# Kernel tuning notes

Hardware: AMD Instinct MI355X
Metric: run time of the kernel (lower is better)

## Reference

```python
import jax, jax.numpy as jnp
import numpy as np

B, NC, H, W, NT = 8, 2048, 128, 128, 4096
EPS = 1e-6


def _off_grid_interp(pts, vals, q):
    """Piecewise-linear scattered interpolation (Delaunay surrogate).
    pts: (Nc,2), vals: (Nc,1), q: (Nt,2) -> (Nt,1).
    For each query, take the 3 nearest context points, compute barycentric
    weights in that triangle; outside/degenerate falls back to mean fill,
    mirroring LinearNDInterpolator(fill_value=vals.mean()).
    """
    d2 = jnp.sum((q[:, None, :] - pts[None, :, :]) ** 2, axis=-1)  # (Nt, Nc)
    _, idx = jax.lax.top_k(-d2, 3)                                  # (Nt, 3)
    tri = pts[idx]                                                  # (Nt, 3, 2)
    tv = vals[idx]                                                  # (Nt, 3, 1)
    p0 = tri[:, 0]
    e1 = tri[:, 1] - p0
    e2 = tri[:, 2] - p0
    r = q - p0
    det = e1[:, 0] * e2[:, 1] - e1[:, 1] * e2[:, 0]
    det_safe = jnp.where(jnp.abs(det) < EPS, 1.0, det)
    w1 = (r[:, 0] * e2[:, 1] - r[:, 1] * e2[:, 0]) / det_safe
    w2 = (e1[:, 0] * r[:, 1] - e1[:, 1] * r[:, 0]) / det_safe
    w0 = 1.0 - w1 - w2
    inside = (w0 >= -EPS) & (w1 >= -EPS) & (w2 >= -EPS) & (jnp.abs(det) >= EPS)
    interp = (w0[:, None] * tv[:, 0] + w1[:, None] * tv[:, 1]
              + w2[:, None] * tv[:, 2])                             # (Nt, 1)
    fill = jnp.mean(vals)
    return jnp.where(inside[:, None], interp, fill)


def _on_grid_interp(grid_x, grid_y, vals, q):
    """Bilinear interpolation on a rectilinear grid (scipy.interpolate.interpn,
    method='linear', bounds_error=False, fill_value=vals.mean()).
    grid_x: (H,), grid_y: (W,), vals: (H,W,1), q: (Nt,2) -> (Nt,1).
    """
    qx, qy = q[:, 0], q[:, 1]
    ix = jnp.clip(jnp.searchsorted(grid_x, qx) - 1, 0, grid_x.shape[0] - 2)
    iy = jnp.clip(jnp.searchsorted(grid_y, qy) - 1, 0, grid_y.shape[0] - 2)
    tx = ((qx - grid_x[ix]) / (grid_x[ix + 1] - grid_x[ix]))[:, None]
    ty = ((qy - grid_y[iy]) / (grid_y[iy + 1] - grid_y[iy]))[:, None]
    v00 = vals[ix, iy]
    v01 = vals[ix, iy + 1]
    v10 = vals[ix + 1, iy]
    v11 = vals[ix + 1, iy + 1]
    interp = (v00 * (1 - tx) * (1 - ty) + v10 * tx * (1 - ty)
              + v01 * (1 - tx) * ty + v11 * tx * ty)
    inside = ((qx >= grid_x[0]) & (qx <= grid_x[-1])
              & (qy >= grid_y[0]) & (qy <= grid_y[-1]))
    fill = jnp.mean(vals)
    return jnp.where(inside[:, None], interp, fill)


def setup_inputs() -> dict:
    key = jax.random.key(0)
    ks = jax.random.split(key, 6)
    xc_off_grid = jax.random.uniform(ks[0], (B, NC, 2), minval=-1.0, maxval=1.0)
    yc_off_grid = jax.random.normal(ks[1], (B, NC, 1))
    gx = jnp.linspace(-1.0, 1.0, H)
    gy = jnp.linspace(-1.0, 1.0, W)
    grid = jnp.stack(jnp.meshgrid(gx, gy, indexing='ij'), axis=-1)  # (H,W,2)
    xc_on_grid = jnp.broadcast_to(grid, (B, H, W, 2))
    yc_on_grid = jax.random.normal(ks[2], (B, H, W, 1))
    xt = jax.random.uniform(ks[3], (B, NT, 2), minval=-1.0, maxval=1.0)
    mix_w = jax.random.normal(ks[4], (2, 1)) * 0.5
    mix_b = jax.random.normal(ks[5], (1,)) * 0.1
    return dict(xc_off_grid=xc_off_grid, yc_off_grid=yc_off_grid,
                xc_on_grid=xc_on_grid, yc_on_grid=yc_on_grid, xt=xt,
                mix_w=mix_w, mix_b=mix_b)


def reference(xc_off_grid, yc_off_grid, xc_on_grid, yc_on_grid, xt, mix_w, mix_b):
    # off-grid scattered interpolation, vmapped over batch
    yt_off = jax.vmap(_off_grid_interp)(xc_off_grid, yc_off_grid, xt)  # (B,Nt,1)
    # on-grid: axis coordinates exactly as the original (bxc_on[:,0,0], bxc_on[0,:,1])
    gx = xc_on_grid[:, :, 0, 0]  # (B, H)
    gy = xc_on_grid[:, 0, :, 1]  # (B, W)
    yt_on = jax.vmap(_on_grid_interp)(gx, gy, yc_on_grid, xt)          # (B,Nt,1)
    yt = jnp.concatenate([yt_off, yt_on], axis=-1)                     # (B,Nt,2)
    return yt @ mix_w + mix_b                                          # (B,Nt,1)
```

## Files before the change

### kernel.cpp

```cpp
#include <hip/hip_runtime.h>
#include <math.h>

#define NB   8
#define NC   2048
#define HH   128
#define WW   128
#define NTQ  4096
#define EPSF 1e-6f
#define CELLW 0.125f
#define BLK  512
#define QPB  64
#define LPQ  8
#define UMAX 0xFFFFFFFFFFFFFFFFULL

typedef unsigned long long u64;

__device__ __forceinline__ void ins3u(u64 u, u64& U0, u64& U1, u64& U2) {
    bool lt2 = u < U2, lt1 = u < U1, lt0 = u < U0;
    U2 = lt1 ? U1 : (lt2 ? u : U2);
    U1 = lt0 ? U0 : (lt1 ? u : U1);
    U0 = lt0 ? u  : U0;
}

__global__ __launch_bounds__(BLK) void fused_interp_kernel(
    const float* __restrict__ xc_off,
    const float* __restrict__ yc_off,
    const float* __restrict__ xc_on,
    const float* __restrict__ yc_on,
    const float* __restrict__ xt,
    const float* __restrict__ mw,
    const float* __restrict__ mb,
    float* __restrict__ out)
{
#pragma clang fp contract(off)
    __shared__ float4 spts[NC];
    __shared__ int    shist[256];
    __shared__ int    soffs[257];
    __shared__ int    scur[256];
    __shared__ float  sgx[HH];
    __shared__ float  sgy[WW];
    __shared__ float  sred[8];
    __shared__ int4   sres[QPB];

    const int tid   = threadIdx.x;
    const int b     = blockIdx.x >> 6;
    const int qbase = (blockIdx.x & 63) * QPB;

    if (tid < 256) shist[tid] = 0;
    const float* xob = xc_on + (size_t)b * HH * WW * 2;
    if (tid >= 256 && tid < 256 + HH) sgx[tid - 256] = xob[(size_t)(tid - 256) * (WW * 2)];
    if (tid >= 384 && tid < 384 + WW) sgy[tid - 384] = xob[2 * (tid - 384) + 1];
    __syncthreads();

    const float2* xcb = (const float2*)(xc_off + (size_t)b * NC * 2);
    const float*  ycb = yc_off + (size_t)b * NC;
    float2 pp_[4]; float vv_[4]; int cc_[4];
    float vsum = 0.f;
#pragma unroll
    for (int t = 0; t < 4; ++t) {
        int k = tid + t * BLK;
        float2 P = xcb[k];
        float  V = ycb[k];
        pp_[t] = P; vv_[t] = V;
        int cx = (int)floorf((P.x + 1.0f) * 8.0f); cx = min(max(cx, 0), 15);
        int cy = (int)floorf((P.y + 1.0f) * 8.0f); cy = min(max(cy, 0), 15);
        cc_[t] = cy * 16 + cx;
        atomicAdd(&shist[cc_[t]], 1);
        vsum += V;
    }
    for (int o = 32; o > 0; o >>= 1) vsum += __shfl_down(vsum, o);
    if ((tid & 63) == 0) sred[tid >> 6] = vsum;
    __syncthreads();

    if (tid < 64) {
        int h0 = shist[4*tid], h1 = shist[4*tid+1], h2 = shist[4*tid+2], h3 = shist[4*tid+3];
        int s = h0 + h1 + h2 + h3; int tot = s;
        for (int off = 1; off < 64; off <<= 1) {
            int u = __shfl_up(s, off);
            if (tid >= off) s += u;
        }
        int excl = s - tot;
        soffs[4*tid]   = excl;
        soffs[4*tid+1] = excl + h0;
        soffs[4*tid+2] = excl + h0 + h1;
        soffs[4*tid+3] = excl + h0 + h1 + h2;
        if (tid == 63) soffs[256] = excl + tot;
    }
    __syncthreads();
    if (tid < 256) scur[tid] = soffs[tid];
    __syncthreads();

#pragma unroll
    for (int t = 0; t < 4; ++t) {
        int k = tid + t * BLK;
        int pos = atomicAdd(&scur[cc_[t]], 1);
        float4 o4; o4.x = pp_[t].x; o4.y = pp_[t].y; o4.z = vv_[t]; o4.w = __int_as_float(k);
        spts[pos] = o4;
    }
    __syncthreads();

    const float fillv = (sred[0] + sred[1] + sred[2] + sred[3] +
                         sred[4] + sred[5] + sred[6] + sred[7]) / (float)NC;

    const int g   = tid & (LPQ - 1);
    const int grp = tid >> 3;
    const int q   = qbase + grp;
    const float2 Q = ((const float2*)xt)[(size_t)b * NTQ + q];
    const float qx = Q.x, qy = Q.y;
    int qcx = (int)floorf((qx + 1.0f) * 8.0f); qcx = min(max(qcx, 0), 15);
    int qcy = (int)floorf((qy + 1.0f) * 8.0f); qcy = min(max(qcy, 0), 15);

    u64 P0 = UMAX, P1 = UMAX, P2 = UMAX;
    u64 F0 = UMAX, F1 = UMAX, F2 = UMAX;

    for (int row = 0; row < 3; ++row) {
        int cy = qcy + row - 1;
        if (cy < 0 || cy > 15) continue;
        int c0 = cy * 16 + max(qcx - 1, 0);
        int c1 = cy * 16 + min(qcx + 1, 15);
        int s = soffs[c0], e = soffs[c1 + 1];
        for (int k = s + g; k < e; k += LPQ) {
            float4 P = spts[k];
            float dx = qx - P.x, dy = qy - P.y;
            float dd = dx * dx + dy * dy;
            u64 u = ((u64)__float_as_uint(dd) << 32) | (unsigned int)__float_as_int(P.w);
            ins3u(u, F0, F1, F2);
        }
    }
    for (int m = 1; m <= 4; m <<= 1) {
        u64 e0 = __shfl_xor(F0, m), e1 = __shfl_xor(F1, m), e2 = __shfl_xor(F2, m);
        ins3u(e0, F0, F1, F2);
        ins3u(e1, F0, F1, F2);
        ins3u(e2, F0, F1, F2);
    }
    P0 = F0; P1 = F1; P2 = F2;

    float bnd = 1.0f * CELLW - 1e-6f;
    u64 thr = ((u64)__float_as_uint(bnd * bnd)) << 32;
    bool done = P2 < thr;

    for (int r = 2; r <= 15; ++r) {
        if (__all(done)) break;
        if (!done) {
            F0 = F1 = F2 = UMAX;
            for (int t = g; t < 8 * r; t += LPQ) {
                int side = t / (2 * r), u = t % (2 * r);
                int dx, dy;
                if (side == 0)      { dx = -r + u; dy = -r; }
                else if (side == 1) { dx = r;      dy = -r + u; }
                else if (side == 2) { dx = r - u;  dy = r; }
                else                { dx = -r;     dy = r - u; }
                int cx = qcx + dx, cy = qcy + dy;
                if (cx < 0 || cx > 15 || cy < 0 || cy > 15) continue;
                int c = cy * 16 + cx;
                int s = soffs[c], e = soffs[c + 1];
                for (int k = s; k < e; ++k) {
                    float4 P = spts[k];
                    float ddx = qx - P.x, ddy = qy - P.y;
                    float dd = ddx * ddx + ddy * ddy;
                    u64 uu = ((u64)__float_as_uint(dd) << 32) | (unsigned int)__float_as_int(P.w);
                    ins3u(uu, F0, F1, F2);
                }
            }
            for (int m = 1; m <= 4; m <<= 1) {
                u64 e0 = __shfl_xor(F0, m), e1 = __shfl_xor(F1, m), e2 = __shfl_xor(F2, m);
                ins3u(e0, F0, F1, F2);
                ins3u(e1, F0, F1, F2);
                ins3u(e2, F0, F1, F2);
            }
            ins3u(F0, P0, P1, P2);
            ins3u(F1, P0, P1, P2);
            ins3u(F2, P0, P1, P2);
            float bb = (float)r * CELLW - 1e-6f;
            u64 tt = ((u64)__float_as_uint(bb * bb)) << 32;
            done = P2 < tt;
        }
    }

    if (g == 0) {
        int4 r4;
        r4.x = (int)(P0 & 0xFFFFFFFFULL);
        r4.y = (int)(P1 & 0xFFFFFFFFULL);
        r4.z = (int)(P2 & 0xFFFFFFFFULL);
        r4.w = 0;
        sres[grp] = r4;
    }
    __syncthreads();

    if (tid < QPB) {
        const int4 r4 = sres[tid];
        const int J0 = r4.x, J1 = r4.y, J2 = r4.z;
        const float2 Qe = ((const float2*)xt)[(size_t)b * NTQ + qbase + tid];
        const float ex = Qe.x, ey = Qe.y;

        float2 A  = xcb[J0];
        float2 Bp = xcb[J1];
        float2 C  = xcb[J2];
        float e1x = Bp.x - A.x, e1y = Bp.y - A.y;
        float e2x = C.x  - A.x, e2y = C.y  - A.y;
        float rx  = ex - A.x,   ry  = ey - A.y;
        float det = e1x * e2y - e1y * e2x;
        float adet = fabsf(det);
        float dets = (adet < EPSF) ? 1.0f : det;
        float w1 = (rx * e2y - ry * e2x) / dets;
        float w2 = (e1x * ry - e1y * rx) / dets;
        float w0 = 1.0f - w1 - w2;
        bool inside = (w0 >= -EPSF) && (w1 >= -EPSF) && (w2 >= -EPSF) && (adet >= EPSF);
        float interp = w0 * ycb[J0] + w1 * ycb[J1] + w2 * ycb[J2];
        float yoff = inside ? interp : fillv;

        int ix = (int)((ex + 1.0f) * 63.5f);
        ix = min(max(ix, 0), HH - 2);
        while (ix > 0 && !(sgx[ix] < ex)) --ix;
        while (ix < HH - 2 && sgx[ix + 1] < ex) ++ix;
        int iy = (int)((ey + 1.0f) * 63.5f);
        iy = min(max(iy, 0), WW - 2);
        while (iy > 0 && !(sgy[iy] < ey)) --iy;
        while (iy < WW - 2 && sgy[iy + 1] < ey) ++iy;

        float x0 = sgx[ix], x1 = sgx[ix + 1];
        float y0 = sgy[iy], y1 = sgy[iy + 1];
        float tx = (ex - x0) / (x1 - x0);
        float ty = (ey - y0) / (y1 - y0);
        const float* yob = yc_on + (size_t)b * HH * WW;
        float v00 = yob[ix * WW + iy];
        float v01 = yob[ix * WW + iy + 1];
        float v10 = yob[(ix + 1) * WW + iy];
        float v11 = yob[(ix + 1) * WW + iy + 1];
        float yon = v00 * (1.f - tx) * (1.f - ty)
                  + v10 * tx * (1.f - ty)
                  + v01 * (1.f - tx) * ty
                  + v11 * tx * ty;

        out[(size_t)b * NTQ + qbase + tid] = yoff * mw[0] + yon * mw[1] + mb[0];
    }
}

extern "C" void kernel_launch(void* const* d_in, const int* in_sizes, int n_in,
                              void* d_out, int out_size, void* d_ws, size_t ws_size,
                              hipStream_t stream) {
    const float* xc_off = (const float*)d_in[0];
    const float* yc_off = (const float*)d_in[1];
    const float* xc_on  = (const float*)d_in[2];
    const float* yc_on  = (const float*)d_in[3];
    const float* xt     = (const float*)d_in[4];
    const float* mix_w  = (const float*)d_in[5];
    const float* mix_b  = (const float*)d_in[6];
    float* out = (float*)d_out;

    fused_interp_kernel<<<NB * (NTQ / QPB), BLK, 0, stream>>>(
        xc_off, yc_off, xc_on, yc_on, xt, mix_w, mix_b, out);
}
```

Baseline: 13.73 us.

## Split grid-binning build into separate kernel, share sorted points via workspace

```diff
diff --git a/kernel.cpp b/kernel.cpp
--- a/kernel.cpp
+++ b/kernel.cpp
@@ -15,6 +15,11 @@
 
 typedef unsigned long long u64;
 
+#define WS_PTS  0
+#define WS_OFF  (NB * NC * 16)
+#define WS_MEAN (WS_OFF + NB * 257 * 4)
+#define WS_NEED (WS_MEAN + NB * 4)
+
 __device__ __forceinline__ void ins3u(u64 u, u64& U0, u64& U1, u64& U2) {
     bool lt2 = u < U2, lt1 = u < U1, lt0 = u < U0;
     U2 = lt1 ? U1 : (lt2 ? u : U2);
@@ -22,43 +27,28 @@
     U0 = lt0 ? u  : U0;
 }
 
-__global__ __launch_bounds__(BLK) void fused_interp_kernel(
-    const float* __restrict__ xc_off,
-    const float* __restrict__ yc_off,
-    const float* __restrict__ xc_on,
-    const float* __restrict__ yc_on,
-    const float* __restrict__ xt,
-    const float* __restrict__ mw,
-    const float* __restrict__ mb,
-    float* __restrict__ out)
+__global__ __launch_bounds__(1024) void build_kernel(
+    const float* __restrict__ xc_off, const float* __restrict__ yc_off,
+    float4* __restrict__ wpts, int* __restrict__ woffs, float* __restrict__ wmean)
 {
-#pragma clang fp contract(off)
     __shared__ float4 spts[NC];
     __shared__ int    shist[256];
     __shared__ int    soffs[257];
     __shared__ int    scur[256];
-    __shared__ float  sgx[HH];
-    __shared__ float  sgy[WW];
-    __shared__ float  sred[8];
-    __shared__ int4   sres[QPB];
-
-    const int tid   = threadIdx.x;
-    const int b     = blockIdx.x >> 6;
-    const int qbase = (blockIdx.x & 63) * QPB;
-
+    __shared__ float  sred[16];
+
+    const int tid = threadIdx.x;
+    const int b   = blockIdx.x;
     if (tid < 256) shist[tid] = 0;
-    const float* xob = xc_on + (size_t)b * HH * WW * 2;
-    if (tid >= 256 && tid < 256 + HH) sgx[tid - 256] = xob[(size_t)(tid - 256) * (WW * 2)];
-    if (tid >= 384 && tid < 384 + WW) sgy[tid - 384] = xob[2 * (tid - 384) + 1];
     __syncthreads();
 
     const float2* xcb = (const float2*)(xc_off + (size_t)b * NC * 2);
     const float*  ycb = yc_off + (size_t)b * NC;
-    float2 pp_[4]; float vv_[4]; int cc_[4];
+    float2 pp_[2]; float vv_[2]; int cc_[2];
     float vsum = 0.f;
 #pragma unroll
-    for (int t = 0; t < 4; ++t) {
-        int k = tid + t * BLK;
+    for (int t = 0; t < 2; ++t) {
+        int k = tid + t * 1024;
         float2 P = xcb[k];
         float  V = ycb[k];
         pp_[t] = P; vv_[t] = V;
@@ -91,16 +81,54 @@
     __syncthreads();
 
 #pragma unroll
-    for (int t = 0; t < 4; ++t) {
-        int k = tid + t * BLK;
+    for (int t = 0; t < 2; ++t) {
+        int k = tid + t * 1024;
         int pos = atomicAdd(&scur[cc_[t]], 1);
         float4 o4; o4.x = pp_[t].x; o4.y = pp_[t].y; o4.z = vv_[t]; o4.w = __int_as_float(k);
         spts[pos] = o4;
     }
     __syncthreads();
 
-    const float fillv = (sred[0] + sred[1] + sred[2] + sred[3] +
-                         sred[4] + sred[5] + sred[6] + sred[7]) / (float)NC;
+#pragma unroll
+    for (int t = 0; t < 2; ++t) {
+        int i = tid + t * 1024;
+        wpts[(size_t)b * NC + i] = spts[i];
+    }
+    if (tid < 257) woffs[b * 257 + tid] = soffs[tid];
+    if (tid == 0) {
+        float s = 0.f;
+        for (int i = 0; i < 16; ++i) s += sred[i];
+        wmean[b] = s / (float)NC;
+    }
+}
+
+__global__ __launch_bounds__(BLK) void search_kernel(
+    const float4* __restrict__ wpts, const int* __restrict__ woffs,
+    const float* __restrict__ wmean,
+    const float* __restrict__ xc_off, const float* __restrict__ yc_off,
+    const float* __restrict__ xc_on,  const float* __restrict__ yc_on,
+    const float* __restrict__ xt, const float* __restrict__ mw,
+    const float* __restrict__ mb, float* __restrict__ out)
+{
+#pragma clang fp contract(off)
+    __shared__ float4 spts[NC];
+    __shared__ int    soffs[257];
+    __shared__ float  sgx[HH];
+    __shared__ float  sgy[WW];
+    __shared__ int4   sres[QPB];
+
+    const int tid   = threadIdx.x;
+    const int b     = blockIdx.x >> 6;
+    const int qbase = (blockIdx.x & 63) * QPB;
+
+    const float4* wp = wpts + (size_t)b * NC;
+#pragma unroll
+    for (int i = tid; i < NC; i += BLK) spts[i] = wp[i];
+    if (tid < 257) soffs[tid] = woffs[b * 257 + tid];
+    const float* xob = xc_on + (size_t)b * HH * WW * 2;
+    if (tid >= 288 && tid < 288 + HH) sgx[tid - 288] = xob[(size_t)(tid - 288) * (WW * 2)];
+    if (tid >= 384 && tid < 384 + WW) sgy[tid - 384] = xob[2 * (tid - 384) + 1];
+    __syncthreads();
 
     const int g   = tid & (LPQ - 1);
     const int grp = tid >> 3;
@@ -188,6 +216,9 @@
     __syncthreads();
 
     if (tid < QPB) {
+        const float fillv = wmean[b];
+        const float2* xcb = (const float2*)(xc_off + (size_t)b * NC * 2);
+        const float*  ycb = yc_off + (size_t)b * NC;
         const int4 r4 = sres[tid];
         const int J0 = r4.x, J1 = r4.y, J2 = r4.z;
         const float2 Qe = ((const float2*)xt)[(size_t)b * NTQ + qbase + tid];
@@ -236,6 +267,188 @@
     }
 }
 
+__global__ __launch_bounds__(BLK) void fused_interp_kernel(
+    const float* __restrict__ xc_off, const float* __restrict__ yc_off,
+    const float* __restrict__ xc_on,  const float* __restrict__ yc_on,
+    const float* __restrict__ xt, const float* __restrict__ mw,
+    const float* __restrict__ mb, float* __restrict__ out)
+{
+#pragma clang fp contract(off)
+    __shared__ float4 spts[NC];
+    __shared__ int    shist[256];
+    __shared__ int    soffs[257];
+    __shared__ int    scur[256];
+    __shared__ float  sgx[HH];
+    __shared__ float  sgy[WW];
+    __shared__ float  sred[8];
+    __shared__ int4   sres[QPB];
+
+    const int tid   = threadIdx.x;
+    const int b     = blockIdx.x >> 6;
+    const int qbase = (blockIdx.x & 63) * QPB;
+
+    if (tid < 256) shist[tid] = 0;
+    const float* xob = xc_on + (size_t)b * HH * WW * 2;
+    if (tid >= 256 && tid < 256 + HH) sgx[tid - 256] = xob[(size_t)(tid - 256) * (WW * 2)];
+    if (tid >= 384 && tid < 384 + WW) sgy[tid - 384] = xob[2 * (tid - 384) + 1];
+    __syncthreads();
+
+    const float2* xcb = (const float2*)(xc_off + (size_t)b * NC * 2);
+    const float*  ycb = yc_off + (size_t)b * NC;
+    float2 pp_[4]; float vv_[4]; int cc_[4];
+    float vsum = 0.f;
+#pragma unroll
+    for (int t = 0; t < 4; ++t) {
+        int k = tid + t * BLK;
+        float2 P = xcb[k]; float V = ycb[k];
+        pp_[t] = P; vv_[t] = V;
+        int cx = (int)floorf((P.x + 1.0f) * 8.0f); cx = min(max(cx, 0), 15);
+        int cy = (int)floorf((P.y + 1.0f) * 8.0f); cy = min(max(cy, 0), 15);
+        cc_[t] = cy * 16 + cx;
+        atomicAdd(&shist[cc_[t]], 1);
+        vsum += V;
+    }
+    for (int o = 32; o > 0; o >>= 1) vsum += __shfl_down(vsum, o);
+    if ((tid & 63) == 0) sred[tid >> 6] = vsum;
+    __syncthreads();
+    if (tid < 64) {
+        int h0 = shist[4*tid], h1 = shist[4*tid+1], h2 = shist[4*tid+2], h3 = shist[4*tid+3];
+        int s = h0 + h1 + h2 + h3; int tot = s;
+        for (int off = 1; off < 64; off <<= 1) {
+            int u = __shfl_up(s, off);
+            if (tid >= off) s += u;
+        }
+        int excl = s - tot;
+        soffs[4*tid] = excl; soffs[4*tid+1] = excl + h0;
+        soffs[4*tid+2] = excl + h0 + h1; soffs[4*tid+3] = excl + h0 + h1 + h2;
+        if (tid == 63) soffs[256] = excl + tot;
+    }
+    __syncthreads();
+    if (tid < 256) scur[tid] = soffs[tid];
+    __syncthreads();
+#pragma unroll
+    for (int t = 0; t < 4; ++t) {
+        int k = tid + t * BLK;
+        int pos = atomicAdd(&scur[cc_[t]], 1);
+        float4 o4; o4.x = pp_[t].x; o4.y = pp_[t].y; o4.z = vv_[t]; o4.w = __int_as_float(k);
+        spts[pos] = o4;
+    }
+    __syncthreads();
+    const float fillv = (sred[0]+sred[1]+sred[2]+sred[3]+sred[4]+sred[5]+sred[6]+sred[7]) / (float)NC;
+
+    const int g = tid & (LPQ - 1);
+    const int grp = tid >> 3;
+    const int q = qbase + grp;
+    const float2 Q = ((const float2*)xt)[(size_t)b * NTQ + q];
+    const float qx = Q.x, qy = Q.y;
+    int qcx = (int)floorf((qx + 1.0f) * 8.0f); qcx = min(max(qcx, 0), 15);
+    int qcy = (int)floorf((qy + 1.0f) * 8.0f); qcy = min(max(qcy, 0), 15);
+    u64 P0 = UMAX, P1 = UMAX, P2 = UMAX, F0 = UMAX, F1 = UMAX, F2 = UMAX;
+    for (int row = 0; row < 3; ++row) {
+        int cy = qcy + row - 1;
+        if (cy < 0 || cy > 15) continue;
+        int c0 = cy * 16 + max(qcx - 1, 0);
+        int c1 = cy * 16 + min(qcx + 1, 15);
+        int s = soffs[c0], e = soffs[c1 + 1];
+        for (int k = s + g; k < e; k += LPQ) {
+            float4 P = spts[k];
+            float dx = qx - P.x, dy = qy - P.y;
+            float dd = dx * dx + dy * dy;
+            u64 u = ((u64)__float_as_uint(dd) << 32) | (unsigned int)__float_as_int(P.w);
+            ins3u(u, F0, F1, F2);
+        }
+    }
+    for (int m = 1; m <= 4; m <<= 1) {
+        u64 e0 = __shfl_xor(F0, m), e1 = __shfl_xor(F1, m), e2 = __shfl_xor(F2, m);
+        ins3u(e0, F0, F1, F2); ins3u(e1, F0, F1, F2); ins3u(e2, F0, F1, F2);
+    }
+    P0 = F0; P1 = F1; P2 = F2;
+    float bnd = 1.0f * CELLW - 1e-6f;
+    u64 thr = ((u64)__float_as_uint(bnd * bnd)) << 32;
+    bool done = P2 < thr;
+    for (int r = 2; r <= 15; ++r) {
+        if (__all(done)) break;
+        if (!done) {
+            F0 = F1 = F2 = UMAX;
+            for (int t = g; t < 8 * r; t += LPQ) {
+                int side = t / (2 * r), u = t % (2 * r);
+                int dx, dy;
+                if (side == 0)      { dx = -r + u; dy = -r; }
+                else if (side == 1) { dx = r;      dy = -r + u; }
+                else if (side == 2) { dx = r - u;  dy = r; }
+                else                { dx = -r;     dy = r - u; }
+                int cx = qcx + dx, cy = qcy + dy;
+                if (cx < 0 || cx > 15 || cy < 0 || cy > 15) continue;
+                int c = cy * 16 + cx;
+                int s = soffs[c], e = soffs[c + 1];
+                for (int k = s; k < e; ++k) {
+                    float4 P = spts[k];
+                    float ddx = qx - P.x, ddy = qy - P.y;
+                    float dd = ddx * ddx + ddy * ddy;
+                    u64 uu = ((u64)__float_as_uint(dd) << 32) | (unsigned int)__float_as_int(P.w);
+                    ins3u(uu, F0, F1, F2);
+                }
+            }
+            for (int m = 1; m <= 4; m <<= 1) {
+                u64 e0 = __shfl_xor(F0, m), e1 = __shfl_xor(F1, m), e2 = __shfl_xor(F2, m);
+                ins3u(e0, F0, F1, F2); ins3u(e1, F0, F1, F2); ins3u(e2, F0, F1, F2);
+            }
+            ins3u(F0, P0, P1, P2); ins3u(F1, P0, P1, P2); ins3u(F2, P0, P1, P2);
+            float bb = (float)r * CELLW - 1e-6f;
+            u64 tt = ((u64)__float_as_uint(bb * bb)) << 32;
+            done = P2 < tt;
+        }
+    }
+    if (g == 0) {
+        int4 r4;
+        r4.x = (int)(P0 & 0xFFFFFFFFULL);
+        r4.y = (int)(P1 & 0xFFFFFFFFULL);
+        r4.z = (int)(P2 & 0xFFFFFFFFULL);
+        r4.w = 0;
+        sres[grp] = r4;
+    }
+    __syncthreads();
+    if (tid < QPB) {
+        const int4 r4 = sres[tid];
+        const int J0 = r4.x, J1 = r4.y, J2 = r4.z;
+        const float2 Qe = ((const float2*)xt)[(size_t)b * NTQ + qbase + tid];
+        const float ex = Qe.x, ey = Qe.y;
+        float2 A = xcb[J0], Bp = xcb[J1], C = xcb[J2];
+        float e1x = Bp.x - A.x, e1y = Bp.y - A.y;
+        float e2x = C.x - A.x, e2y = C.y - A.y;
+        float rx = ex - A.x, ry = ey - A.y;
+        float det = e1x * e2y - e1y * e2x;
+        float adet = fabsf(det);
+        float dets = (adet < EPSF) ? 1.0f : det;
+        float w1 = (rx * e2y - ry * e2x) / dets;
+        float w2 = (e1x * ry - e1y * rx) / dets;
+        float w0 = 1.0f - w1 - w2;
+        bool inside = (w0 >= -EPSF) && (w1 >= -EPSF) && (w2 >= -EPSF) && (adet >= EPSF);
+        float interp = w0 * ycb[J0] + w1 * ycb[J1] + w2 * ycb[J2];
+        float yoff = inside ? interp : fillv;
+        int ix = (int)((ex + 1.0f) * 63.5f);
+        ix = min(max(ix, 0), HH - 2);
+        while (ix > 0 && !(sgx[ix] < ex)) --ix;
+        while (ix < HH - 2 && sgx[ix + 1] < ex) ++ix;
+        int iy = (int)((ey + 1.0f) * 63.5f);
+        iy = min(max(iy, 0), WW - 2);
+        while (iy > 0 && !(sgy[iy] < ey)) --iy;
+        while (iy < WW - 2 && sgy[iy + 1] < ey) ++iy;
+        float x0 = sgx[ix], x1 = sgx[ix + 1];
+        float y0 = sgy[iy], y1 = sgy[iy + 1];
+        float tx = (ex - x0) / (x1 - x0);
+        float ty = (ey - y0) / (y1 - y0);
+        const float* yob = yc_on + (size_t)b * HH * WW;
+        float v00 = yob[ix * WW + iy];
+        float v01 = yob[ix * WW + iy + 1];
+        float v10 = yob[(ix + 1) * WW + iy];
+        float v11 = yob[(ix + 1) * WW + iy + 1];
+        float yon = v00 * (1.f - tx) * (1.f - ty) + v10 * tx * (1.f - ty)
+                  + v01 * (1.f - tx) * ty + v11 * tx * ty;
+        out[(size_t)b * NTQ + qbase + tid] = yoff * mw[0] + yon * mw[1] + mb[0];
+    }
+}
+
 extern "C" void kernel_launch(void* const* d_in, const int* in_sizes, int n_in,
                               void* d_out, int out_size, void* d_ws, size_t ws_size,
                               hipStream_t stream) {
@@ -248,6 +461,15 @@
     const float* mix_b  = (const float*)d_in[6];
     float* out = (float*)d_out;
 
-    fused_interp_kernel<<<NB * (NTQ / QPB), BLK, 0, stream>>>(
-        xc_off, yc_off, xc_on, yc_on, xt, mix_w, mix_b, out);
+    if (ws_size >= (size_t)WS_NEED) {
+        float4* wpts  = (float4*)((char*)d_ws + WS_PTS);
+        int*    woffs = (int*)((char*)d_ws + WS_OFF);
+        float*  wmean = (float*)((char*)d_ws + WS_MEAN);
+        build_kernel<<<NB, 1024, 0, stream>>>(xc_off, yc_off, wpts, woffs, wmean);
+        search_kernel<<<NB * (NTQ / QPB), BLK, 0, stream>>>(
+            wpts, woffs, wmean, xc_off, yc_off, xc_on, yc_on, xt, mix_w, mix_b, out);
+    } else {
+        fused_interp_kernel<<<NB * (NTQ / QPB), BLK, 0, stream>>>(
+            xc_off, yc_off, xc_on, yc_on, xt, mix_w, mix_b, out);
+    }
 }
```

Measured after the change: 17.54 us. 1.28x slower.
